# Performance work log

Measured on AMD Instinct MI355X. Metric: run time of the kernel, lower is better.

## Reference

```python
import jax, jax.numpy as jnp
import numpy as np

T, B, N = 1000, 64, 512
DT = 0.01
EL, VR, TR, TINF = -0.07, -0.07, -0.06, -0.05
A_VAL = 2.6239240169525146
A1_VAL = -0.015625353902578354
A2_VAL = -1.0590057373046875
B_VAL = 12.77495288848877
G_VAL = 45.24007797241211
K1, K2 = 200.0, 20.0
R1, R2 = 0.3858567178249359, -1.1421641111373901
C = 1.0


def setup_inputs() -> dict:
    key = jax.random.key(0)
    x = jax.random.normal(key, (T, B, N), dtype=jnp.float32)
    linear = jnp.ones((1, N), jnp.float32)
    a = jnp.full((1, N), A_VAL, jnp.float32)
    A1 = jnp.full((1, N), A1_VAL * C, jnp.float32)
    A2 = jnp.full((1, N), A2_VAL * C, jnp.float32)
    return {"x": x, "linear": linear, "a": a, "A1": A1, "A2": A2}


def _spike(v):
    # Heaviside step (forward of SurrGradSpike)
    return (v > 0).astype(v.dtype)


def reference(x, linear, a, A1, A2):
    G = G_VAL * C

    def step(state, xt):
        V, i1, i2, Thr = state
        i1 = i1 - K1 * i1 * DT
        i2 = i2 - K2 * i2 * DT
        V = V + DT * (linear * xt + i1 + i2 - G * (V - EL)) / C
        Thr = Thr + DT * (a * (V - EL) - B_VAL * (Thr - TINF))
        spk = _spike(V - Thr)
        i1 = (1.0 - spk) * i1 + spk * (R1 * i1 + A1)
        i2 = (1.0 - spk) * i2 + spk * (R2 * i2 + A2)
        Thr = (1.0 - spk) * Thr + spk * jnp.maximum(Thr, TR)
        V = (1.0 - spk) * V + spk * VR
        return (V, i1, i2, Thr), spk

    Bd, Nd = x.shape[1], x.shape[2]
    init = (
        jnp.full((Bd, Nd), EL, x.dtype),   # V
        jnp.zeros((Bd, Nd), x.dtype),      # i1
        jnp.zeros((Bd, Nd), x.dtype),      # i2
        jnp.full((Bd, Nd), TINF, x.dtype), # Thr
    )
    _, spikes = jax.lax.scan(step, init, x)
    return spikes  # [T, B, N] (original returns np.array of per-step spikes)
```

## Files before the change

kernel.cpp:

```cpp
#include <hip/hip_runtime.h>


#define T_STEPS 1000
#define B_DIM 64
#define N_DIM 512
#define BN (B_DIM * N_DIM)

#define K_CHUNK 20
#define NCHUNK (T_STEPS / K_CHUNK)

#define C_DT   0.01f
#define C_EL   (-0.07f)
#define C_VR   (-0.07f)
#define C_TR   (-0.06f)
#define C_TINF (-0.05f)
#define C_B    12.77495288848877f
#define C_G    45.24007797241211f
#define C_K1   200.0f
#define C_K2   20.0f
#define C_R1   0.3858567178249359f
#define C_R2   (-1.1421641111373901f)

typedef const __attribute__((address_space(1))) void* gp_t;
typedef __attribute__((address_space(3))) void* lp_t;

__device__ __forceinline__ float mn_step(float xt, float lin, float av,
                                         float A1v, float A2v,
                                         float& V, float& i1, float& i2,
                                         float& Thr)
{
#pragma clang fp contract(off)
    i1 = i1 - (C_K1 * i1) * C_DT;
    i2 = i2 - (C_K2 * i2) * C_DT;
    float p  = lin * xt;
    float q  = p + i1;
    float r  = q + i2;
    float e  = V - C_EL;
    float g  = C_G * e;
    float s  = r - g;
    float d  = C_DT * s;
    V = V + d;
    float e2 = V - C_EL;
    float u  = av * e2;
    float w  = Thr - C_TINF;
    float bw = C_B * w;
    float s2 = u - bw;
    float d2 = C_DT * s2;
    Thr = Thr + d2;
    float diff = V - Thr;
    bool  sb   = diff > 0.0f;
    float spk  = sb ? 1.0f : 0.0f;
    float i1r = (C_R1 * i1) + A1v;
    float i2r = (C_R2 * i2) + A2v;
    i1  = sb ? i1r : i1;
    i2  = sb ? i2r : i2;
    float tm = fmaxf(Thr, C_TR);
    Thr = sb ? tm : Thr;
    V   = sb ? C_VR : V;
    return spk;
}

__global__ __launch_bounds__(128) void mn_neuron_kernel(
    const float* __restrict__ x, const float* __restrict__ linear,
    const float* __restrict__ a, const float* __restrict__ A1,
    const float* __restrict__ A2, float* __restrict__ out)
{
#pragma clang fp contract(off)
    __shared__ float lds[2][K_CHUNK][64];

    const int lane = threadIdx.x & 63;
    const int wid  = threadIdx.x >> 6;
    const int blk  = blockIdx.x;

    if (wid == 1) {
        const float* pl = x + (size_t)(lane >> 4) * BN
                            + (size_t)blk * 64 + (size_t)(lane & 15) * 4;

        {
#pragma unroll
            for (int s = 0; s < K_CHUNK / 4; ++s) {
                __builtin_amdgcn_global_load_lds(
                    (gp_t)(pl + (size_t)(s * 4) * BN),
                    (lp_t)&lds[0][s * 4][0], 16, 0, 0);
            }
            __builtin_amdgcn_s_waitcnt(0x0F70);
        }
        __syncthreads();

        for (int c = 0; c < NCHUNK; ++c) {
            if (c + 1 < NCHUNK) {
                const float* pc = pl + (size_t)((c + 1) * K_CHUNK) * BN;
                float* dst = &lds[(c + 1) & 1][0][0];
#pragma unroll
                for (int s = 0; s < K_CHUNK / 4; ++s) {
                    __builtin_amdgcn_global_load_lds(
                        (gp_t)(pc + (size_t)(s * 4) * BN),
                        (lp_t)(dst + s * 4 * 64), 16, 0, 0);
                }
                __builtin_amdgcn_s_waitcnt(0x0F70);
            }
            __syncthreads();
        }
    } else {
        const int idx = blk * 64 + lane;
        const int n   = idx & (N_DIM - 1);

        const float lin = linear[n];
        const float av  = a[n];
        const float A1v = A1[n];
        const float A2v = A2[n];

        float V   = C_EL;
        float i1  = 0.0f;
        float i2  = 0.0f;
        float Thr = C_TINF;

        float* op = out + idx;

        __syncthreads();

        for (int c = 0; c < NCHUNK; ++c) {
            const float* src = &lds[c & 1][0][lane];
#pragma unroll
            for (int j = 0; j < K_CHUNK; ++j) {
                float xt  = src[j * 64];
                float spk = mn_step(xt, lin, av, A1v, A2v, V, i1, i2, Thr);
                *op = spk;
                op += BN;
            }
            __syncthreads();
        }
    }
}

extern "C" void kernel_launch(void* const* d_in, const int* in_sizes, int n_in,
                              void* d_out, int out_size, void* d_ws, size_t ws_size,
                              hipStream_t stream) {
    const float* x      = (const float*)d_in[0];
    const float* linear = (const float*)d_in[1];
    const float* a      = (const float*)d_in[2];
    const float* A1     = (const float*)d_in[3];
    const float* A2     = (const float*)d_in[4];
    float* out = (float*)d_out;

    mn_neuron_kernel<<<BN / 64, 128, 0, stream>>>(x, linear, a, A1, A2, out);
}
```

Baseline: 233.5 us.

## Replace producer-wave LDS pipeline with per-thread register prefetch ring

Drops the dedicated loader wavefront, the LDS double buffer and the per-chunk block barriers. Each thread now prefetches its own next chunk of 20 inputs into registers while it computes the current chunk, and launches 64-thread blocks. Output stores become nontemporal. This removes synchronisation and LDS traffic, but relies on per-thread 4-byte loads with no async DMA and uses more registers.

```diff
diff --git a/kernel.cpp b/kernel.cpp
--- a/kernel.cpp
+++ b/kernel.cpp
@@ -20,9 +20,6 @@
 #define C_K2   20.0f
 #define C_R1   0.3858567178249359f
 #define C_R2   (-1.1421641111373901f)
-
-typedef const __attribute__((address_space(1))) void* gp_t;
-typedef __attribute__((address_space(3))) void* lp_t;
 
 __device__ __forceinline__ float mn_step(float xt, float lin, float av,
                                          float A1v, float A2v,
@@ -60,76 +57,54 @@
     return spk;
 }
 
-__global__ __launch_bounds__(128) void mn_neuron_kernel(
+__global__ __launch_bounds__(64) void mn_neuron_kernel(
     const float* __restrict__ x, const float* __restrict__ linear,
     const float* __restrict__ a, const float* __restrict__ A1,
     const float* __restrict__ A2, float* __restrict__ out)
 {
 #pragma clang fp contract(off)
-    __shared__ float lds[2][K_CHUNK][64];
+    const int lane = threadIdx.x;
+    const int idx  = blockIdx.x * 64 + lane;
+    const int n    = idx & (N_DIM - 1);
 
-    const int lane = threadIdx.x & 63;
-    const int wid  = threadIdx.x >> 6;
-    const int blk  = blockIdx.x;
+    const float lin = linear[n];
+    const float av  = a[n];
+    const float A1v = A1[n];
+    const float A2v = A2[n];
 
-    if (wid == 1) {
-        const float* pl = x + (size_t)(lane >> 4) * BN
-                            + (size_t)blk * 64 + (size_t)(lane & 15) * 4;
+    float V   = C_EL;
+    float i1  = 0.0f;
+    float i2  = 0.0f;
+    float Thr = C_TINF;
 
-        {
+    const float* xp = x + idx;
+    float*       op = out + idx;
+
+    float xb[K_CHUNK];
+
 #pragma unroll
-            for (int s = 0; s < K_CHUNK / 4; ++s) {
-                __builtin_amdgcn_global_load_lds(
-                    (gp_t)(pl + (size_t)(s * 4) * BN),
-                    (lp_t)&lds[0][s * 4][0], 16, 0, 0);
-            }
-            __builtin_amdgcn_s_waitcnt(0x0F70);
+    for (int j = 0; j < K_CHUNK; ++j)
+        xb[j] = xp[(size_t)j * BN];
+    xp += (size_t)K_CHUNK * BN;
+
+    for (int c = 0; c < NCHUNK - 1; ++c) {
+#pragma unroll
+        for (int j = 0; j < K_CHUNK; ++j) {
+            float xt = xb[j];
+            xb[j] = xp[(size_t)j * BN];
+            float spk = mn_step(xt, lin, av, A1v, A2v, V, i1, i2, Thr);
+            __builtin_nontemporal_store(spk, op);
+            op += BN;
         }
-        __syncthreads();
+        xp += (size_t)K_CHUNK * BN;
+    }
 
-        for (int c = 0; c < NCHUNK; ++c) {
-            if (c + 1 < NCHUNK) {
-                const float* pc = pl + (size_t)((c + 1) * K_CHUNK) * BN;
-                float* dst = &lds[(c + 1) & 1][0][0];
 #pragma unroll
-                for (int s = 0; s < K_CHUNK / 4; ++s) {
-                    __builtin_amdgcn_global_load_lds(
-                        (gp_t)(pc + (size_t)(s * 4) * BN),
-                        (lp_t)(dst + s * 4 * 64), 16, 0, 0);
-                }
-                __builtin_amdgcn_s_waitcnt(0x0F70);
-            }
-            __syncthreads();
-        }
-    } else {
-        const int idx = blk * 64 + lane;
-        const int n   = idx & (N_DIM - 1);
-
-        const float lin = linear[n];
-        const float av  = a[n];
-        const float A1v = A1[n];
-        const float A2v = A2[n];
-
-        float V   = C_EL;
-        float i1  = 0.0f;
-        float i2  = 0.0f;
-        float Thr = C_TINF;
-
-        float* op = out + idx;
-
-        __syncthreads();
-
-        for (int c = 0; c < NCHUNK; ++c) {
-            const float* src = &lds[c & 1][0][lane];
-#pragma unroll
-            for (int j = 0; j < K_CHUNK; ++j) {
-                float xt  = src[j * 64];
-                float spk = mn_step(xt, lin, av, A1v, A2v, V, i1, i2, Thr);
-                *op = spk;
-                op += BN;
-            }
-            __syncthreads();
-        }
+    for (int j = 0; j < K_CHUNK; ++j) {
+        float xt  = xb[j];
+        float spk = mn_step(xt, lin, av, A1v, A2v, V, i1, i2, Thr);
+        __builtin_nontemporal_store(spk, op);
+        op += BN;
     }
 }
 
@@ -143,5 +118,5 @@
     const float* A2     = (const float*)d_in[4];
     float* out = (float*)d_out;
 
-    mn_neuron_kernel<<<BN / 64, 128, 0, stream>>>(x, linear, a, A1, A2, out);
+    mn_neuron_kernel<<<BN / 64, 64, 0, stream>>>(x, linear, a, A1, A2, out);
 }
```

Result: slower. 273.6 us (+17.2%).
